# Optimization experiments

Hardware: AMD Instinct MI355X
Metric: run time of the kernel (lower is better)

## Reference

```python
import jax, jax.numpy as jnp
import numpy as np

B, N, H, O = 2, 512, 128, 32  # batch, n_particles, hidden_dim, obs_dim


def _linear_init(key, out_d, in_d):
    kw, kb = jax.random.split(key)
    s = 1.0 / np.sqrt(in_d)
    W = jax.random.uniform(kw, (out_d, in_d), minval=-s, maxval=s, dtype=jnp.float32)
    b = jax.random.uniform(kb, (out_d,), minval=-s, maxval=s, dtype=jnp.float32)
    return W, b


def setup_inputs() -> dict:
    key = jax.random.key(0)
    ks = jax.random.split(key, 8)
    z = jax.random.normal(ks[0], (B, N, H), dtype=jnp.float32)
    s_t = jax.random.normal(ks[1], (B, N, O), dtype=jnp.float32)
    W1, b1 = _linear_init(ks[2], H, 2 * H)   # relation_mlp layer 0
    W2, b2 = _linear_init(ks[3], H, H)       # relation_mlp layer 2
    Wq, bq = _linear_init(ks[4], H, H)       # query_proj
    Wk, bk = _linear_init(ks[5], H, O)       # key_proj
    W3, b3 = _linear_init(ks[6], H, H)       # aggregation_mlp layer 0
    W4, b4 = _linear_init(ks[7], H, H)       # aggregation_mlp layer 2
    return dict(z=z, s_t=s_t, W1=W1, b1=b1, W2=W2, b2=b2, Wq=Wq, bq=bq,
                Wk=Wk, bk=bk, W3=W3, b3=b3, W4=W4, b4=b4)


def reference(z, s_t, W1, b1, W2, b2, Wq, bq, Wk, bk, W3, b3, W4, b4):
    b_, n, h = z.shape
    # query depends only on i, key only on j (repeat in the original is redundant)
    q = z @ Wq.T + bq            # [B,N,H]
    k = s_t @ Wk.T + bk          # [B,N,H]
    scores = jnp.einsum('bih,bjh->bij', q, k) / (h ** 0.5)   # [B,N,N]
    eye = jnp.eye(n, dtype=bool)
    scores = jnp.where(eye, -jnp.inf, scores)
    attn = jax.nn.softmax(scores, axis=-1)                   # [B,N,N]
    # relation_mlp on concat(z_i, z_j): split first weight into i- and j- halves
    W1i, W1j = W1[:, :h], W1[:, h:]
    zi = z @ W1i.T               # [B,N,H]
    zj = z @ W1j.T               # [B,N,H]
    rel = jnp.tanh(zi[:, :, None, :] + zj[:, None, :, :] + b1) @ W2.T + b2  # [B,N,N,H]
    agg = jnp.einsum('bij,bijh->bih', attn, rel)             # weighted sum over j
    dz_dt = jnp.tanh(agg @ W3.T + b3) @ W4.T + b4
    return dz_dt
```

## Files before the change

kernel.cpp:

```cpp
#include <hip/hip_runtime.h>
#include <hip/hip_bf16.h>

#define NN 512
#define HH 128
#define OO 32

#define KL 2.8853900817779268f

__device__ __forceinline__ float vexp2(float x) {
    float r; asm("v_exp_f32 %0, %1" : "=v"(r) : "v"(x)); return r;
}
__device__ __forceinline__ float vrcp(float x) {
    float r; asm("v_rcp_f32 %0, %1" : "=v"(r) : "v"(x)); return r;
}
__device__ __forceinline__ float tanh_fast(float x) {
    float e = vexp2(KL * x);
    return 1.0f - 2.0f * vrcp(e + 1.0f);
}
__device__ __forceinline__ float waveRedSum(float v) {
#pragma unroll
    for (int off = 32; off > 0; off >>= 1) v += __shfl_xor(v, off, 64);
    return v;
}
__device__ __forceinline__ float red8(float v) {
    v += __shfl_xor(v, 1, 64); v += __shfl_xor(v, 2, 64); v += __shfl_xor(v, 4, 64);
    return v;
}
__device__ __forceinline__ float dot16r(const float4* w, const float* x, int rot) {
    float a = 0;
#pragma unroll
    for (int ii = 0; ii < 4; ii++) {
        int i = (ii + rot) & 3;
        float4 xv = *(const float4*)(x + i * 4);
        a = fmaf(xv.x, w[ii].x, a); a = fmaf(xv.y, w[ii].y, a);
        a = fmaf(xv.z, w[ii].z, a); a = fmaf(xv.w, w[ii].w, a);
    }
    return a;
}
__device__ __forceinline__ unsigned short f2bf(float x) {
    unsigned u = __float_as_uint(x);
    u += 0x7fffu + ((u >> 16) & 1u);
    return (unsigned short)(u >> 16);
}
__device__ __forceinline__ float bf_lo(unsigned u) { return __uint_as_float((u & 0xffffu) << 16); }
__device__ __forceinline__ float bf_hi(unsigned u) { return __uint_as_float(u & 0xffff0000u); }

__global__ __launch_bounds__(1024, 4) void prep_kernel(
    const float* __restrict__ z, const float* __restrict__ s_t,
    const float* __restrict__ W1, const float* __restrict__ b1,
    const float* __restrict__ Wq, const float* __restrict__ bq,
    const float* __restrict__ Wk, const float* __restrict__ bk,
    float* __restrict__ qP, float* __restrict__ cP,
    unsigned short* __restrict__ EzjG, unsigned* __restrict__ kTp) {
    __shared__ float zrow[4][HH];
    __shared__ float srow[4][OO];
    int t = threadIdx.x, bid = blockIdx.x;
    int r0 = bid * 4, b = bid >> 7, i0 = (bid & 127) * 4;
    int kq = t & 7, h = t >> 3, rot = (kq >> 1) & 3;

    const float4* WqP = (const float4*)(Wq + (size_t)h * HH) + kq * 4;
    const float4* WiP = (const float4*)(W1 + (size_t)h * 2 * HH) + kq * 4;
    const float4* WjP = (const float4*)(W1 + (size_t)h * 2 * HH + HH) + kq * 4;
    float4 wq[4], wi[4], wj[4];
#pragma unroll
    for (int ii = 0; ii < 4; ii++) {
        wq[ii] = WqP[(ii + rot) & 3];
        wi[ii] = WiP[(ii + rot) & 3];
        wj[ii] = WjP[(ii + rot) & 3];
    }
    float4 wk = ((const float4*)(Wk + (size_t)h * OO))[kq];
    float vbq = bq[h], vb1 = b1[h], vbk = bk[h];

    if (t < 4 * HH) zrow[t >> 7][t & 127] = z[(size_t)r0 * HH + t];
    else if (t < 4 * HH + 4 * OO) {
        int u = t - 4 * HH;
        srow[u >> 5][u & 31] = s_t[(size_t)r0 * OO + u];
    }
    __syncthreads();

    {
        float a0 = red8(dot16r(wq, &zrow[0][kq * 16], rot));
        float a1 = red8(dot16r(wq, &zrow[1][kq * 16], rot));
        float a2 = red8(dot16r(wq, &zrow[2][kq * 16], rot));
        float a3 = red8(dot16r(wq, &zrow[3][kq * 16], rot));
        if (kq == 0) {
            float* qp = qP + (size_t)bid * 512 + h * 4;
            qp[0] = a0 + vbq; qp[1] = a1 + vbq; qp[2] = a2 + vbq; qp[3] = a3 + vbq;
        }
    }
    {
        float a0 = red8(dot16r(wi, &zrow[0][kq * 16], rot));
        float a1 = red8(dot16r(wi, &zrow[1][kq * 16], rot));
        float a2 = red8(dot16r(wi, &zrow[2][kq * 16], rot));
        float a3 = red8(dot16r(wi, &zrow[3][kq * 16], rot));
        if (kq == 0) {
            float* cp = cP + (size_t)bid * 512 + h * 4;
            cp[0] = vexp2(KL * (a0 + vb1)); cp[1] = vexp2(KL * (a1 + vb1));
            cp[2] = vexp2(KL * (a2 + vb1)); cp[3] = vexp2(KL * (a3 + vb1));
        }
    }
    {
        float a0 = red8(dot16r(wj, &zrow[0][kq * 16], rot));
        float a1 = red8(dot16r(wj, &zrow[1][kq * 16], rot));
        float a2 = red8(dot16r(wj, &zrow[2][kq * 16], rot));
        float a3 = red8(dot16r(wj, &zrow[3][kq * 16], rot));
        if (kq == 0) {
            EzjG[(size_t)(r0 + 0) * HH + h] = f2bf(vexp2(KL * a0));
            EzjG[(size_t)(r0 + 1) * HH + h] = f2bf(vexp2(KL * a1));
            EzjG[(size_t)(r0 + 2) * HH + h] = f2bf(vexp2(KL * a2));
            EzjG[(size_t)(r0 + 3) * HH + h] = f2bf(vexp2(KL * a3));
        }
    }
    {
        float4 s0 = *(const float4*)&srow[0][kq * 4];
        float4 s1 = *(const float4*)&srow[1][kq * 4];
        float4 s2 = *(const float4*)&srow[2][kq * 4];
        float4 s3 = *(const float4*)&srow[3][kq * 4];
        float a0 = red8(s0.x * wk.x + s0.y * wk.y + s0.z * wk.z + s0.w * wk.w);
        float a1 = red8(s1.x * wk.x + s1.y * wk.y + s1.z * wk.z + s1.w * wk.w);
        float a2 = red8(s2.x * wk.x + s2.y * wk.y + s2.z * wk.z + s2.w * wk.w);
        float a3 = red8(s3.x * wk.x + s3.y * wk.y + s3.z * wk.z + s3.w * wk.w);
        if (kq == 0) {
            unsigned p01 = (unsigned)f2bf(a0 + vbk) | ((unsigned)f2bf(a1 + vbk) << 16);
            unsigned p23 = (unsigned)f2bf(a2 + vbk) | ((unsigned)f2bf(a3 + vbk) << 16);
            unsigned* kp = kTp + ((size_t)b * HH + h) * 256 + (i0 >> 1);
            kp[0] = p01; kp[1] = p23;
        }
    }
}

__global__ __launch_bounds__(1024, 4) void fused_kernel(
    const float* __restrict__ qP, const float* __restrict__ cP,
    const unsigned* __restrict__ kTp, const unsigned short* __restrict__ EzjG,
    const float* __restrict__ W2, const float* __restrict__ b2,
    const float* __restrict__ W3, const float* __restrict__ b3,
    const float* __restrict__ W4, const float* __restrict__ b4,
    float* __restrict__ out) {
    __shared__ float q4T[HH][4];
    __shared__ float c4T[HH][4];
    __shared__ float attnR[4][NN];
    __shared__ float buf[8192];
    __shared__ float UL[4][HH];
    __shared__ float aggL[4][HH];
    __shared__ float h1L[4][HH];
    __shared__ float redA[16];
    __shared__ float invS[4];

    float2 (*scp)[4][256] = (float2 (*)[4][256])buf;
    float (*part)[4][HH] = (float (*)[4][HH])buf;

    int t = threadIdx.x, bid = blockIdx.x;
    int b = bid >> 7, i0 = (bid & 127) * 4, r0 = bid * 4;

    if (t < 512) ((float*)q4T)[t] = qP[(size_t)bid * 512 + t];
    else         ((float*)c4T)[t - 512] = cP[(size_t)bid * 512 + (t - 512)];
    __syncthreads();

    {
        int jp = t & 255, hq = t >> 8, h0 = hq * 32;
        const unsigned* kb = kTp + ((size_t)b * HH + h0) * 256 + jp;
        float s0l = 0, s1l = 0, s2l = 0, s3l = 0;
        float s0h = 0, s1h = 0, s2h = 0, s3h = 0;
#pragma unroll 8
        for (int hh = 0; hh < 32; hh++) {
            unsigned u = kb[(size_t)hh * 256];
            float kl = bf_lo(u), kh = bf_hi(u);
            float4 qv = *(const float4*)q4T[h0 + hh];
            s0l = fmaf(qv.x, kl, s0l); s1l = fmaf(qv.y, kl, s1l);
            s2l = fmaf(qv.z, kl, s2l); s3l = fmaf(qv.w, kl, s3l);
            s0h = fmaf(qv.x, kh, s0h); s1h = fmaf(qv.y, kh, s1h);
            s2h = fmaf(qv.z, kh, s2h); s3h = fmaf(qv.w, kh, s3h);
        }
        scp[hq][0][jp] = make_float2(s0l, s0h);
        scp[hq][1][jp] = make_float2(s1l, s1h);
        scp[hq][2][jp] = make_float2(s2l, s2h);
        scp[hq][3][jp] = make_float2(s3l, s3h);
    }
    __syncthreads();

    {
        int jp = t & 255, r = t >> 8;
        float sl = 0, sh = 0;
#pragma unroll
        for (int hq = 0; hq < 4; hq++) {
            float2 v = scp[hq][r][jp];
            sl += v.x; sh += v.y;
        }
        const float sc = 0.08838834764831845f;
        float el = __expf(sl * sc), eh = __expf(sh * sc);
        int jl = 2 * jp;
        if (jl == i0 + r)     el = 0.0f;
        if (jl + 1 == i0 + r) eh = 0.0f;
        *(float2*)&attnR[r][jl] = make_float2(el, eh);
        float ps = waveRedSum(el + eh);
        int lane = t & 63, w = t >> 6;
        if (lane == 0) redA[w] = ps;
    }
    __syncthreads();
    if (t < 4) {
        float S = redA[t * 4] + redA[t * 4 + 1] + redA[t * 4 + 2] + redA[t * 4 + 3];
        invS[t] = __fdividef(1.0f, S);
    }

    {
        int lane6 = t & 63, qs = t >> 6, hp = lane6 * 2, jb = qs * 32;
        const unsigned* zbU = (const unsigned*)EzjG + (size_t)b * NN * 64 + lane6;
        float4 cA = *(const float4*)c4T[hp];
        float4 cB = *(const float4*)c4T[hp + 1];
        float a0A = 0, a1A = 0, a2A = 0, a3A = 0;
        float a0B = 0, a1B = 0, a2B = 0, a3B = 0;
#pragma unroll 8
        for (int jj = 0; jj < 32; jj++) {
            int jc = jb + jj;
            unsigned u = zbU[(size_t)jc * 64];
            float Ex = bf_lo(u), Ey = bf_hi(u);
            float w0 = attnR[0][jc], w1 = attnR[1][jc];
            float w2 = attnR[2][jc], w3 = attnR[3][jc];
            a0A = fmaf(w0, vrcp(fmaf(cA.x, Ex, 1.0f)), a0A);
            a1A = fmaf(w1, vrcp(fmaf(cA.y, Ex, 1.0f)), a1A);
            a2A = fmaf(w2, vrcp(fmaf(cA.z, Ex, 1.0f)), a2A);
            a3A = fmaf(w3, vrcp(fmaf(cA.w, Ex, 1.0f)), a3A);
            a0B = fmaf(w0, vrcp(fmaf(cB.x, Ey, 1.0f)), a0B);
            a1B = fmaf(w1, vrcp(fmaf(cB.y, Ey, 1.0f)), a1B);
            a2B = fmaf(w2, vrcp(fmaf(cB.z, Ey, 1.0f)), a2B);
            a3B = fmaf(w3, vrcp(fmaf(cB.w, Ey, 1.0f)), a3B);
        }
        *(float2*)&part[qs][0][hp] = make_float2(a0A, a0B);
        *(float2*)&part[qs][1][hp] = make_float2(a1A, a1B);
        *(float2*)&part[qs][2][hp] = make_float2(a2A, a2B);
        *(float2*)&part[qs][3][hp] = make_float2(a3A, a3B);
    }
    __syncthreads();
    if (t < 512) {
        int r = t >> 7, h = t & 127;
        float s = 0;
#pragma unroll
        for (int q = 0; q < 16; q++) s += part[q][r][h];
        UL[r][h] = fmaf(-2.0f * invS[r], s, 1.0f);
    }
    __syncthreads();

    {
        int kq = t & 7, h8 = t >> 3, rot = (kq >> 1) & 3;
        float4 w[4];
        {
            const float4* Wp = (const float4*)(W2 + (size_t)h8 * HH) + kq * 4;
#pragma unroll
            for (int ii = 0; ii < 4; ii++) w[ii] = Wp[(ii + rot) & 3];
            float a0 = red8(dot16r(w, &UL[0][kq * 16], rot));
            float a1 = red8(dot16r(w, &UL[1][kq * 16], rot));
            float a2 = red8(dot16r(w, &UL[2][kq * 16], rot));
            float a3 = red8(dot16r(w, &UL[3][kq * 16], rot));
            if (kq == 0) {
                float vb = b2[h8];
                aggL[0][h8] = a0 + vb; aggL[1][h8] = a1 + vb;
                aggL[2][h8] = a2 + vb; aggL[3][h8] = a3 + vb;
            }
        }
        __syncthreads();
        {
            const float4* Wp = (const float4*)(W3 + (size_t)h8 * HH) + kq * 4;
#pragma unroll
            for (int ii = 0; ii < 4; ii++) w[ii] = Wp[(ii + rot) & 3];
            float a0 = red8(dot16r(w, &aggL[0][kq * 16], rot));
            float a1 = red8(dot16r(w, &aggL[1][kq * 16], rot));
            float a2 = red8(dot16r(w, &aggL[2][kq * 16], rot));
            float a3 = red8(dot16r(w, &aggL[3][kq * 16], rot));
            if (kq == 0) {
                float vb = b3[h8];
                h1L[0][h8] = tanh_fast(a0 + vb); h1L[1][h8] = tanh_fast(a1 + vb);
                h1L[2][h8] = tanh_fast(a2 + vb); h1L[3][h8] = tanh_fast(a3 + vb);
            }
        }
        __syncthreads();
        {
            const float4* Wp = (const float4*)(W4 + (size_t)h8 * HH) + kq * 4;
#pragma unroll
            for (int ii = 0; ii < 4; ii++) w[ii] = Wp[(ii + rot) & 3];
            float a0 = red8(dot16r(w, &h1L[0][kq * 16], rot));
            float a1 = red8(dot16r(w, &h1L[1][kq * 16], rot));
            float a2 = red8(dot16r(w, &h1L[2][kq * 16], rot));
            float a3 = red8(dot16r(w, &h1L[3][kq * 16], rot));
            if (kq == 0) {
                float vb = b4[h8];
                out[(size_t)(r0 + 0) * HH + h8] = a0 + vb;
                out[(size_t)(r0 + 1) * HH + h8] = a1 + vb;
                out[(size_t)(r0 + 2) * HH + h8] = a2 + vb;
                out[(size_t)(r0 + 3) * HH + h8] = a3 + vb;
            }
        }
    }
}

extern "C" void kernel_launch(void* const* d_in, const int* in_sizes, int n_in,
                              void* d_out, int out_size, void* d_ws, size_t ws_size,
                              hipStream_t stream) {
    const float* z   = (const float*)d_in[0];
    const float* s_t = (const float*)d_in[1];
    const float* W1  = (const float*)d_in[2];
    const float* b1  = (const float*)d_in[3];
    const float* W2  = (const float*)d_in[4];
    const float* b2  = (const float*)d_in[5];
    const float* Wq  = (const float*)d_in[6];
    const float* bq  = (const float*)d_in[7];
    const float* Wk  = (const float*)d_in[8];
    const float* bk  = (const float*)d_in[9];
    const float* W3  = (const float*)d_in[10];
    const float* b3  = (const float*)d_in[11];
    const float* W4  = (const float*)d_in[12];
    const float* b4  = (const float*)d_in[13];
    float* out = (float*)d_out;

    float* ws = (float*)d_ws;
    unsigned* kTp = (unsigned*)ws;
    float* qP = ws + 65536;
    float* cP = ws + 196608;
    unsigned short* Ezj = (unsigned short*)(ws + 327680);

    hipLaunchKernelGGL(prep_kernel, dim3(256), dim3(1024), 0, stream,
                       z, s_t, W1, b1, Wq, bq, Wk, bk, qP, cP, Ezj, kTp);
    hipLaunchKernelGGL(fused_kernel, dim3(256), dim3(1024), 0, stream,
                       qP, cP, kTp, Ezj, W2, b2, W3, b3, W4, b4, out);
}
```

Before: 34.16 us.

## Make score, softmax and aggregation wave-local to remove block barriers

Remaps the score computation so each wave owns 32 consecutive j columns, with the four h-quarters split across lanes and reduced by shuffles instead of through shared memory. Each wave then writes its own exp weights and partial softmax sums to wave-private shared slices and consumes them immediately in the aggregation loop over the same j range. This removes two block-wide barriers and the separate partial-score and reduction passes. The normalizer is folded into the final per-row reduction. The cost is 8-way redundant exp work per j pair, and eBuf is read by the same wave without a wave-level barrier, which relies on implicit ordering of LDS accesses within a wave.

```diff
diff --git a/kernel.cpp b/kernel.cpp
--- a/kernel.cpp
+++ b/kernel.cpp
@@ -16,11 +16,6 @@
 __device__ __forceinline__ float tanh_fast(float x) {
     float e = vexp2(KL * x);
     return 1.0f - 2.0f * vrcp(e + 1.0f);
-}
-__device__ __forceinline__ float waveRedSum(float v) {
-#pragma unroll
-    for (int off = 32; off > 0; off >>= 1) v += __shfl_xor(v, off, 64);
-    return v;
 }
 __device__ __forceinline__ float red8(float v) {
     v += __shfl_xor(v, 1, 64); v += __shfl_xor(v, 2, 64); v += __shfl_xor(v, 4, 64);
@@ -138,26 +133,24 @@
     float* __restrict__ out) {
     __shared__ float q4T[HH][4];
     __shared__ float c4T[HH][4];
-    __shared__ float attnR[4][NN];
-    __shared__ float buf[8192];
+    __shared__ float eBuf[16][4][32];
+    __shared__ float sliceS[16][4];
+    __shared__ float part[16][4][HH];
     __shared__ float UL[4][HH];
     __shared__ float aggL[4][HH];
     __shared__ float h1L[4][HH];
-    __shared__ float redA[16];
-    __shared__ float invS[4];
-
-    float2 (*scp)[4][256] = (float2 (*)[4][256])buf;
-    float (*part)[4][HH] = (float (*)[4][HH])buf;
 
     int t = threadIdx.x, bid = blockIdx.x;
     int b = bid >> 7, i0 = (bid & 127) * 4, r0 = bid * 4;
+    int w = t >> 6, lane = t & 63;
 
     if (t < 512) ((float*)q4T)[t] = qP[(size_t)bid * 512 + t];
     else         ((float*)c4T)[t - 512] = cP[(size_t)bid * 512 + (t - 512)];
     __syncthreads();
 
     {
-        int jp = t & 255, hq = t >> 8, h0 = hq * 32;
+        int jp_local = lane & 15, hq = lane >> 4;
+        int jp = w * 16 + jp_local, h0 = hq * 32;
         const unsigned* kb = kTp + ((size_t)b * HH + h0) * 256 + jp;
         float s0l = 0, s1l = 0, s2l = 0, s3l = 0;
         float s0h = 0, s1h = 0, s2h = 0, s3h = 0;
@@ -171,51 +164,55 @@
             s0h = fmaf(qv.x, kh, s0h); s1h = fmaf(qv.y, kh, s1h);
             s2h = fmaf(qv.z, kh, s2h); s3h = fmaf(qv.w, kh, s3h);
         }
-        scp[hq][0][jp] = make_float2(s0l, s0h);
-        scp[hq][1][jp] = make_float2(s1l, s1h);
-        scp[hq][2][jp] = make_float2(s2l, s2h);
-        scp[hq][3][jp] = make_float2(s3l, s3h);
-    }
-    __syncthreads();
-
-    {
-        int jp = t & 255, r = t >> 8;
-        float sl = 0, sh = 0;
-#pragma unroll
-        for (int hq = 0; hq < 4; hq++) {
-            float2 v = scp[hq][r][jp];
-            sl += v.x; sh += v.y;
-        }
+        s0l += __shfl_xor(s0l, 16, 64); s0l += __shfl_xor(s0l, 32, 64);
+        s1l += __shfl_xor(s1l, 16, 64); s1l += __shfl_xor(s1l, 32, 64);
+        s2l += __shfl_xor(s2l, 16, 64); s2l += __shfl_xor(s2l, 32, 64);
+        s3l += __shfl_xor(s3l, 16, 64); s3l += __shfl_xor(s3l, 32, 64);
+        s0h += __shfl_xor(s0h, 16, 64); s0h += __shfl_xor(s0h, 32, 64);
+        s1h += __shfl_xor(s1h, 16, 64); s1h += __shfl_xor(s1h, 32, 64);
+        s2h += __shfl_xor(s2h, 16, 64); s2h += __shfl_xor(s2h, 32, 64);
+        s3h += __shfl_xor(s3h, 16, 64); s3h += __shfl_xor(s3h, 32, 64);
+
         const float sc = 0.08838834764831845f;
-        float el = __expf(sl * sc), eh = __expf(sh * sc);
-        int jl = 2 * jp;
-        if (jl == i0 + r)     el = 0.0f;
-        if (jl + 1 == i0 + r) eh = 0.0f;
-        *(float2*)&attnR[r][jl] = make_float2(el, eh);
-        float ps = waveRedSum(el + eh);
-        int lane = t & 63, w = t >> 6;
-        if (lane == 0) redA[w] = ps;
-    }
-    __syncthreads();
-    if (t < 4) {
-        float S = redA[t * 4] + redA[t * 4 + 1] + redA[t * 4 + 2] + redA[t * 4 + 3];
-        invS[t] = __fdividef(1.0f, S);
-    }
-
-    {
-        int lane6 = t & 63, qs = t >> 6, hp = lane6 * 2, jb = qs * 32;
-        const unsigned* zbU = (const unsigned*)EzjG + (size_t)b * NN * 64 + lane6;
+        float e0l = __expf(s0l * sc), e1l = __expf(s1l * sc);
+        float e2l = __expf(s2l * sc), e3l = __expf(s3l * sc);
+        float e0h = __expf(s0h * sc), e1h = __expf(s1h * sc);
+        float e2h = __expf(s2h * sc), e3h = __expf(s3h * sc);
+        int jl = jp * 2, jh = jl + 1;
+        if (jl == i0 + 0) e0l = 0.0f;  if (jh == i0 + 0) e0h = 0.0f;
+        if (jl == i0 + 1) e1l = 0.0f;  if (jh == i0 + 1) e1h = 0.0f;
+        if (jl == i0 + 2) e2l = 0.0f;  if (jh == i0 + 2) e2h = 0.0f;
+        if (jl == i0 + 3) e3l = 0.0f;  if (jh == i0 + 3) e3h = 0.0f;
+
+        float ts0 = e0l + e0h, ts1 = e1l + e1h, ts2 = e2l + e2h, ts3 = e3l + e3h;
+#pragma unroll
+        for (int m = 1; m <= 8; m <<= 1) {
+            ts0 += __shfl_xor(ts0, m, 64); ts1 += __shfl_xor(ts1, m, 64);
+            ts2 += __shfl_xor(ts2, m, 64); ts3 += __shfl_xor(ts3, m, 64);
+        }
+        if (lane == 0) {
+            sliceS[w][0] = ts0; sliceS[w][1] = ts1;
+            sliceS[w][2] = ts2; sliceS[w][3] = ts3;
+        }
+        if (hq == 0) {
+            *(float2*)&eBuf[w][0][2 * jp_local] = make_float2(e0l, e0h);
+            *(float2*)&eBuf[w][1][2 * jp_local] = make_float2(e1l, e1h);
+            *(float2*)&eBuf[w][2][2 * jp_local] = make_float2(e2l, e2h);
+            *(float2*)&eBuf[w][3][2 * jp_local] = make_float2(e3l, e3h);
+        }
+
+        int hp = lane * 2, jb = w * 32;
+        const unsigned* zbU = (const unsigned*)EzjG + (size_t)b * NN * 64 + lane;
         float4 cA = *(const float4*)c4T[hp];
         float4 cB = *(const float4*)c4T[hp + 1];
         float a0A = 0, a1A = 0, a2A = 0, a3A = 0;
         float a0B = 0, a1B = 0, a2B = 0, a3B = 0;
 #pragma unroll 8
         for (int jj = 0; jj < 32; jj++) {
-            int jc = jb + jj;
-            unsigned u = zbU[(size_t)jc * 64];
+            unsigned u = zbU[(size_t)(jb + jj) * 64];
             float Ex = bf_lo(u), Ey = bf_hi(u);
-            float w0 = attnR[0][jc], w1 = attnR[1][jc];
-            float w2 = attnR[2][jc], w3 = attnR[3][jc];
+            float w0 = eBuf[w][0][jj], w1 = eBuf[w][1][jj];
+            float w2 = eBuf[w][2][jj], w3 = eBuf[w][3][jj];
             a0A = fmaf(w0, vrcp(fmaf(cA.x, Ex, 1.0f)), a0A);
             a1A = fmaf(w1, vrcp(fmaf(cA.y, Ex, 1.0f)), a1A);
             a2A = fmaf(w2, vrcp(fmaf(cA.z, Ex, 1.0f)), a2A);
@@ -225,32 +222,33 @@
             a2B = fmaf(w2, vrcp(fmaf(cB.z, Ey, 1.0f)), a2B);
             a3B = fmaf(w3, vrcp(fmaf(cB.w, Ey, 1.0f)), a3B);
         }
-        *(float2*)&part[qs][0][hp] = make_float2(a0A, a0B);
-        *(float2*)&part[qs][1][hp] = make_float2(a1A, a1B);
-        *(float2*)&part[qs][2][hp] = make_float2(a2A, a2B);
-        *(float2*)&part[qs][3][hp] = make_float2(a3A, a3B);
+        *(float2*)&part[w][0][hp] = make_float2(a0A, a0B);
+        *(float2*)&part[w][1][hp] = make_float2(a1A, a1B);
+        *(float2*)&part[w][2][hp] = make_float2(a2A, a2B);
+        *(float2*)&part[w][3][hp] = make_float2(a3A, a3B);
     }
     __syncthreads();
+
     if (t < 512) {
         int r = t >> 7, h = t & 127;
-        float s = 0;
-#pragma unroll
-        for (int q = 0; q < 16; q++) s += part[q][r][h];
-        UL[r][h] = fmaf(-2.0f * invS[r], s, 1.0f);
+        float s = 0, S = 0;
+#pragma unroll
+        for (int q = 0; q < 16; q++) { s += part[q][r][h]; S += sliceS[q][r]; }
+        UL[r][h] = fmaf(-2.0f * vrcp(S), s, 1.0f);
     }
     __syncthreads();
 
     {
         int kq = t & 7, h8 = t >> 3, rot = (kq >> 1) & 3;
-        float4 w[4];
+        float4 wv[4];
         {
             const float4* Wp = (const float4*)(W2 + (size_t)h8 * HH) + kq * 4;
 #pragma unroll
-            for (int ii = 0; ii < 4; ii++) w[ii] = Wp[(ii + rot) & 3];
-            float a0 = red8(dot16r(w, &UL[0][kq * 16], rot));
-            float a1 = red8(dot16r(w, &UL[1][kq * 16], rot));
-            float a2 = red8(dot16r(w, &UL[2][kq * 16], rot));
-            float a3 = red8(dot16r(w, &UL[3][kq * 16], rot));
+            for (int ii = 0; ii < 4; ii++) wv[ii] = Wp[(ii + rot) & 3];
+            float a0 = red8(dot16r(wv, &UL[0][kq * 16], rot));
+            float a1 = red8(dot16r(wv, &UL[1][kq * 16], rot));
+            float a2 = red8(dot16r(wv, &UL[2][kq * 16], rot));
+            float a3 = red8(dot16r(wv, &UL[3][kq * 16], rot));
             if (kq == 0) {
                 float vb = b2[h8];
                 aggL[0][h8] = a0 + vb; aggL[1][h8] = a1 + vb;
@@ -261,11 +259,11 @@
         {
             const float4* Wp = (const float4*)(W3 + (size_t)h8 * HH) + kq * 4;
 #pragma unroll
-            for (int ii = 0; ii < 4; ii++) w[ii] = Wp[(ii + rot) & 3];
-            float a0 = red8(dot16r(w, &aggL[0][kq * 16], rot));
-            float a1 = red8(dot16r(w, &aggL[1][kq * 16], rot));
-            float a2 = red8(dot16r(w, &aggL[2][kq * 16], rot));
-            float a3 = red8(dot16r(w, &aggL[3][kq * 16], rot));
+            for (int ii = 0; ii < 4; ii++) wv[ii] = Wp[(ii + rot) & 3];
+            float a0 = red8(dot16r(wv, &aggL[0][kq * 16], rot));
+            float a1 = red8(dot16r(wv, &aggL[1][kq * 16], rot));
+            float a2 = red8(dot16r(wv, &aggL[2][kq * 16], rot));
+            float a3 = red8(dot16r(wv, &aggL[3][kq * 16], rot));
             if (kq == 0) {
                 float vb = b3[h8];
                 h1L[0][h8] = tanh_fast(a0 + vb); h1L[1][h8] = tanh_fast(a1 + vb);
@@ -276,11 +274,11 @@
         {
             const float4* Wp = (const float4*)(W4 + (size_t)h8 * HH) + kq * 4;
 #pragma unroll
-            for (int ii = 0; ii < 4; ii++) w[ii] = Wp[(ii + rot) & 3];
-            float a0 = red8(dot16r(w, &h1L[0][kq * 16], rot));
-            float a1 = red8(dot16r(w, &h1L[1][kq * 16], rot));
-            float a2 = red8(dot16r(w, &h1L[2][kq * 16], rot));
-            float a3 = red8(dot16r(w, &h1L[3][kq * 16], rot));
+            for (int ii = 0; ii < 4; ii++) wv[ii] = Wp[(ii + rot) & 3];
+            float a0 = red8(dot16r(wv, &h1L[0][kq * 16], rot));
+            float a1 = red8(dot16r(wv, &h1L[1][kq * 16], rot));
+            float a2 = red8(dot16r(wv, &h1L[2][kq * 16], rot));
+            float a3 = red8(dot16r(wv, &h1L[3][kq * 16], rot));
             if (kq == 0) {
                 float vb = b4[h8];
                 out[(size_t)(r0 + 0) * HH + h8] = a0 + vb;
```

After: 34.52 us. No clear change (+1.1%).
